# Kernel optimization log

Measured on AMD Instinct MI355X. Metric: run time of the kernel, lower is better.

## Reference

```python
import jax, jax.numpy as jnp
import numpy as np

B, T, C = 4, 2048, 1024
H = 16
D = C // H  # head_dim = 64


def setup_inputs() -> dict:
    key = jax.random.key(0)
    k1, k2, k3, k4, k5 = jax.random.split(key, 5)
    s = 1.0 / np.sqrt(C)
    return {
        "x": jax.random.normal(k1, (B, T, C), dtype=jnp.float32),
        "Wqkv": jax.random.normal(k2, (C, 3 * C), dtype=jnp.float32) * s,
        "bqkv": jax.random.normal(k3, (3 * C,), dtype=jnp.float32) * 0.02,
        "Wproj": jax.random.normal(k4, (C, C), dtype=jnp.float32) * s,
        "bproj": jax.random.normal(k5, (C,), dtype=jnp.float32) * 0.02,
    }


def reference(x, Wqkv, bqkv, Wproj, bproj):
    b, t, c = x.shape
    qkv = x @ Wqkv + bqkv                      # [B,T,3C]
    qkv = qkv.reshape(b, t, 3, H, D)
    q, k, v = (qkv[:, :, i].transpose(0, 2, 1, 3) for i in range(3))  # [B,H,T,D]
    scale = D ** -0.5
    attn = jnp.einsum("bhqd,bhkd->bhqk", q, k) * scale
    causal = jnp.tril(jnp.ones((t, t), dtype=bool))
    attn = jnp.where(causal[None, None], attn, -jnp.inf)
    attn = jax.nn.softmax(attn, axis=-1)
    out = jnp.einsum("bhqk,bhkd->bhqd", attn, v)  # [B,H,T,D]
    out = out.transpose(0, 2, 1, 3).reshape(b, t, c)
    return out @ Wproj + bproj
```

## Files before the change

### kernel.cpp

```cpp
#include <hip/hip_runtime.h>
#include <hip/hip_bf16.h>

typedef __bf16 bf16;
typedef __bf16 bf16x4 __attribute__((ext_vector_type(4)));
typedef __bf16 bf16x8 __attribute__((ext_vector_type(8)));
typedef float  f32x4  __attribute__((ext_vector_type(4)));

#define DEV static __device__ __forceinline__

static constexpr int Bsz = 4, T = 2048, C = 1024, H = 16;
static constexpr int M  = Bsz * T;
static constexpr int N1 = 3 * C;
static constexpr float SM_SCALE = 0.125f;

DEV void gload16(const bf16* g, const bf16* l) {
  __builtin_amdgcn_global_load_lds(
      (const __attribute__((address_space(1))) void*)g,
      (__attribute__((address_space(3))) void*)l, 16, 0, 0);
}

__launch_bounds__(256)
__global__ void convert_kernel(const float* __restrict__ in, bf16* __restrict__ out) {
  const size_t i = ((size_t)blockIdx.x * 256 + threadIdx.x) * 8;
  f32x4 a = *(const f32x4*)(in + i);
  f32x4 b = *(const f32x4*)(in + i + 4);
  *(bf16x4*)(out + i)     = __builtin_convertvector(a, bf16x4);
  *(bf16x4*)(out + i + 4) = __builtin_convertvector(b, bf16x4);
}

__launch_bounds__(256)
__global__ void transpose_conv_kernel(const float* __restrict__ in,
                                      bf16* __restrict__ out, int K, int N) {
  __shared__ float t[32][33];
  const int n0 = blockIdx.x * 32, k0 = blockIdx.y * 32;
  const int tx = threadIdx.x & 31, ty = threadIdx.x >> 5;
#pragma unroll
  for (int j = 0; j < 4; ++j)
    t[ty + j * 8][tx] = in[(size_t)(k0 + ty + j * 8) * N + n0 + tx];
  __syncthreads();
#pragma unroll
  for (int j = 0; j < 4; ++j)
    out[(size_t)(n0 + ty + j * 8) * K + k0 + tx] = (bf16)t[tx][ty + j * 8];
}

template <bool OUT_BF16, bool V_SPLIT>
__launch_bounds__(512, 1)
__global__ void gemm8_kernel(const bf16* __restrict__ A,
                             const bf16* __restrict__ Bt,
                             const float* __restrict__ bias,
                             void* __restrict__ Out, bf16* __restrict__ vt,
                             int Ndim, int Kdim) {
  __shared__ bf16 ldsA[3][128 * 64];
  __shared__ bf16 ldsB[3][256 * 64];
  const int tid = threadIdx.x, l = tid & 63, w = tid >> 6;
  const int wm = w >> 2, wn = w & 3;
  const int lr = l & 15, lh = l >> 4;
  const int m0 = blockIdx.x * 128, n0 = blockIdx.y * 256;
  const int rA = tid >> 3, cA = tid & 7;
  const int cs = cA ^ (rA & 7);

  auto STAGE = [&](int nb, int t) {
    const int k0 = t * 64;
#pragma unroll
    for (int i = 0; i < 2; ++i) {
      const int row = i * 64 + rA;
      gload16(A + (size_t)(m0 + row) * Kdim + k0 + cs * 8,
              &ldsA[nb][i * 4096 + w * 512]);
    }
#pragma unroll
    for (int i = 0; i < 4; ++i) {
      const int row = i * 64 + rA;
      gload16(Bt + (size_t)(n0 + row) * Kdim + k0 + cs * 8,
              &ldsB[nb][i * 4096 + w * 512]);
    }
  };

  f32x4 acc[4][4] = {};
  const int NT = Kdim >> 6;

  STAGE(0, 0);
  STAGE(1, 1);
  asm volatile("s_waitcnt vmcnt(6)" ::: "memory");
  __builtin_amdgcn_sched_barrier(0);
  __builtin_amdgcn_s_barrier();
  __builtin_amdgcn_sched_barrier(0);

  for (int t = 0; t < NT; ++t) {
    const int cur = t % 3;
    const bool more = (t + 2) < NT;
    if (more) STAGE((t + 2) % 3, t + 2);
    __builtin_amdgcn_sched_barrier(0);

    const bf16* a_ = &ldsA[cur][0];
    const bf16* b_ = &ldsB[cur][0];
    bf16x8 af[2][4], bfm[2][4];
#pragma unroll
    for (int kk = 0; kk < 2; ++kk) {
#pragma unroll
      for (int mi = 0; mi < 4; ++mi) {
        const int row = wm * 64 + mi * 16 + lr;
        af[kk][mi] = *(const bf16x8*)&a_[row * 64 + (((kk * 4 + lh) ^ (row & 7)) << 3)];
      }
#pragma unroll
      for (int ni = 0; ni < 4; ++ni) {
        const int row = wn * 64 + ni * 16 + lr;
        bfm[kk][ni] = *(const bf16x8*)&b_[row * 64 + (((kk * 4 + lh) ^ (row & 7)) << 3)];
      }
    }
    __builtin_amdgcn_s_setprio(1);
#pragma unroll
    for (int kk = 0; kk < 2; ++kk)
#pragma unroll
      for (int mi = 0; mi < 4; ++mi)
#pragma unroll
        for (int ni = 0; ni < 4; ++ni)
          acc[mi][ni] = __builtin_amdgcn_mfma_f32_16x16x32_bf16(
              af[kk][mi], bfm[kk][ni], acc[mi][ni], 0, 0, 0);
    __builtin_amdgcn_s_setprio(0);
    __builtin_amdgcn_sched_barrier(0);

    if (t + 1 < NT) {
      if (more) {
        asm volatile("s_waitcnt vmcnt(6)" ::: "memory");
      } else {
        asm volatile("s_waitcnt vmcnt(0)" ::: "memory");
      }
      __builtin_amdgcn_sched_barrier(0);
      __builtin_amdgcn_s_barrier();
      __builtin_amdgcn_sched_barrier(0);
    }
  }

  if (V_SPLIT && n0 >= 2 * C) {
    const int b = m0 >> 11, tb = (m0 & 2047) + wm * 64;
#pragma unroll
    for (int ni = 0; ni < 4; ++ni) {
      const int col = n0 - 2 * C + wn * 64 + ni * 16 + lr;
      const int hh = col >> 6, dd = col & 63;
      const float bv = bias[2 * C + col];
      bf16* vdst = vt + ((size_t)((b * H + hh) * 64 + dd)) * T + tb + lh * 4;
#pragma unroll
      for (int mi = 0; mi < 4; ++mi) {
        bf16x4 p4;
#pragma unroll
        for (int r = 0; r < 4; ++r) p4[r] = (bf16)(acc[mi][ni][r] + bv);
        *(bf16x4*)&vdst[mi * 16] = p4;
      }
    }
  } else {
#pragma unroll
    for (int ni = 0; ni < 4; ++ni) {
      const int col = n0 + wn * 64 + ni * 16 + lr;
      const float bv = bias[col];
#pragma unroll
      for (int mi = 0; mi < 4; ++mi) {
#pragma unroll
        for (int r = 0; r < 4; ++r) {
          const int row = m0 + wm * 64 + mi * 16 + lh * 4 + r;
          const float v = acc[mi][ni][r] + bv;
          if (OUT_BF16)
            ((bf16*)Out)[(size_t)row * Ndim + col] = (bf16)v;
          else
            ((float*)Out)[(size_t)row * Ndim + col] = v;
        }
      }
    }
  }
}

DEV int vswz3(int d) { return (d & 7) ^ ((d >> 3) & 7); }

__launch_bounds__(512, 4)
__global__ void attn_kernel(const bf16* __restrict__ qk,
                            const bf16* __restrict__ vt,
                            bf16* __restrict__ out) {
  __shared__ bf16 lds_k[2][128 * 64];
  __shared__ bf16 lds_vt[2][64 * 128];
  __shared__ bf16 lds_p[8][16 * 64];
  const int tid = threadIdx.x, l = tid & 63, w = tid >> 6;
  const int lr = l & 15, lh = l >> 4;
  const int p = blockIdx.x;
  const int bh = p >> 3, jj = p & 7;
  const int b = bh >> 4, h = bh & 15;
  const size_t RS = 2 * C;
  const bf16* base  = qk + (size_t)b * T * RS;
  const bf16* kbase = base + C + h * 64;
  const bf16* vth   = vt + (size_t)bh * 64 * T;
  bf16* op = out + (size_t)b * T * C + h * 64;
  const int r1 = tid >> 3, cc = tid & 7;
  const int kc = cc ^ (r1 & 7);
  const int dV = tid >> 4, cV = tid & 15;

  auto STAGE = [&](int nb, int kt) {
#pragma unroll
    for (int i = 0; i < 2; ++i) {
      const int rowK = i * 64 + r1;
      gload16(kbase + (size_t)(kt * 128 + rowK) * RS + kc * 8,
              &lds_k[nb][i * 4096 + w * 512]);
      const int d = i * 32 + dV;
      const int vc = (cV & 8) | (((cV & 7) ^ vswz3(d)) & 7);
      gload16(vth + (size_t)d * T + kt * 128 + vc * 8,
              &lds_vt[nb][i * 4096 + w * 512]);
    }
  };

  for (int it = 0; it < 2; ++it) {
    const int J = it ? jj : 15 - jj;
    const int q16 = J * 128 + w * 16;
    bf16x8 qf[2];
#pragma unroll
    for (int kk = 0; kk < 2; ++kk) {
      bf16x8 qv = *(const bf16x8*)(base + (size_t)(q16 + lr) * RS + h * 64 + kk * 32 + lh * 8);
#pragma unroll
      for (int j = 0; j < 8; ++j) qf[kk][j] = (bf16)((float)qv[j] * SM_SCALE);
    }

    float mq = -__builtin_inff(), lq = 0.f;
    f32x4 o[4] = {};

    __syncthreads();
    STAGE(0, 0);
    __syncthreads();

    int buf = 0;
    for (int kt = 0; kt <= J; ++kt) {
      const bf16* kb = &lds_k[buf][0];
      const bf16* vb = &lds_vt[buf][0];
      if (kt < J) STAGE(buf ^ 1, kt + 1);

      f32x4 s8[8] = {};
      __builtin_amdgcn_s_setprio(1);
#pragma unroll
      for (int kk = 0; kk < 2; ++kk) {
#pragma unroll
        for (int kn = 0; kn < 8; ++kn) {
          const int key = kn * 16 + lr;
          bf16x8 kf = *(const bf16x8*)&kb[(key * 64 + kk * 32 + lh * 8) ^ ((key & 7) << 3)];
          s8[kn] = __builtin_amdgcn_mfma_f32_16x16x32_bf16(kf, qf[kk], s8[kn], 0, 0, 0);
        }
      }
      __builtin_amdgcn_s_setprio(0);
      if (kt == J) {
        const int qloc = w * 16 + lr;
#pragma unroll
        for (int kn = 0; kn < 8; ++kn)
#pragma unroll
          for (int r = 0; r < 4; ++r)
            if ((kn * 16 + lh * 4 + r) > qloc) s8[kn][r] = -__builtin_inff();
      }
      float pm = s8[0][0];
#pragma unroll
      for (int kn = 0; kn < 8; ++kn)
#pragma unroll
        for (int r = 0; r < 4; ++r) pm = fmaxf(pm, s8[kn][r]);
      pm = fmaxf(pm, __shfl_xor(pm, 16));
      pm = fmaxf(pm, __shfl_xor(pm, 32));
      const float mnew = fmaxf(mq, pm);
      const float alpha_q = __expf(mq - mnew);
      mq = mnew;
      float ssum = 0.f;
#pragma unroll
      for (int kn = 0; kn < 8; ++kn)
#pragma unroll
        for (int r = 0; r < 4; ++r) {
          const float p2 = __expf(s8[kn][r] - mnew);
          s8[kn][r] = p2;
          ssum += p2;
        }
      ssum += __shfl_xor(ssum, 16);
      ssum += __shfl_xor(ssum, 32);
      lq = lq * alpha_q + ssum;
      float al[4];
#pragma unroll
      for (int r = 0; r < 4; ++r) al[r] = __shfl(alpha_q, lh * 4 + r);
#pragma unroll
      for (int ni = 0; ni < 4; ++ni)
#pragma unroll
        for (int r = 0; r < 4; ++r) o[ni][r] *= al[r];
#pragma unroll
      for (int hh = 0; hh < 2; ++hh) {
#pragma unroll
        for (int kn4 = 0; kn4 < 4; ++kn4) {
          const int kn = hh * 4 + kn4;
          bf16x4 pb;
#pragma unroll
          for (int r = 0; r < 4; ++r) pb[r] = (bf16)s8[kn][r];
          *(bf16x4*)&lds_p[w][(lr * 64 + kn4 * 16 + lh * 4) ^ ((lr & 7) << 3)] = pb;
        }
        __builtin_amdgcn_s_setprio(1);
#pragma unroll
        for (int kkl = 0; kkl < 2; ++kkl) {
          bf16x8 pf = *(const bf16x8*)&lds_p[w][(lr * 64 + kkl * 32 + lh * 8) ^ ((lr & 7) << 3)];
#pragma unroll
          for (int ni = 0; ni < 4; ++ni) {
            const int d = ni * 16 + lr;
            const int key = hh * 64 + kkl * 32 + lh * 8;
            bf16x8 vf = *(const bf16x8*)&vb[d * 128 + (key ^ (vswz3(d) << 3))];
            o[ni] = __builtin_amdgcn_mfma_f32_16x16x32_bf16(pf, vf, o[ni], 0, 0, 0);
          }
        }
        __builtin_amdgcn_s_setprio(0);
      }

      if (kt < J) {
        __syncthreads();
        buf ^= 1;
      }
    }
    float lrec[4];
#pragma unroll
    for (int r = 0; r < 4; ++r) lrec[r] = 1.0f / __shfl(lq, lh * 4 + r);
#pragma unroll
    for (int ni = 0; ni < 4; ++ni)
#pragma unroll
      for (int r = 0; r < 4; ++r) {
        const int qrow = q16 + lh * 4 + r;
        op[(size_t)qrow * C + ni * 16 + lr] = (bf16)(o[ni][r] * lrec[r]);
      }
  }
}

extern "C" void kernel_launch(void* const* d_in, const int* in_sizes, int n_in,
                              void* d_out, int out_size, void* d_ws, size_t ws_size,
                              hipStream_t stream) {
  const float* x     = (const float*)d_in[0];
  const float* Wqkv  = (const float*)d_in[1];
  const float* bqkv  = (const float*)d_in[2];
  const float* Wproj = (const float*)d_in[3];
  const float* bproj = (const float*)d_in[4];
  float* out = (float*)d_out;

  char* ws = (char*)d_ws;
  bf16* qk       = (bf16*)(ws);
  bf16* vt       = (bf16*)(ws + 33554432);
  bf16* wqkvt    = (bf16*)(ws + 50331648);
  bf16* wprojt   = (bf16*)(ws + 56623104);
  bf16* attn_out = (bf16*)(ws + 58720256);
  bf16* x_bf16   = attn_out;

  convert_kernel<<<dim3(M * C / (256 * 8)), 256, 0, stream>>>(x, x_bf16);
  transpose_conv_kernel<<<dim3(N1 / 32, C / 32), 256, 0, stream>>>(Wqkv, wqkvt, C, N1);
  transpose_conv_kernel<<<dim3(C / 32, C / 32), 256, 0, stream>>>(Wproj, wprojt, C, C);
  gemm8_kernel<true, true><<<dim3(M / 128, N1 / 256), 512, 0, stream>>>(
      x_bf16, wqkvt, bqkv, qk, vt, 2 * C, C);
  attn_kernel<<<dim3(Bsz * H * 8), 512, 0, stream>>>(qk, vt, attn_out);
  gemm8_kernel<false, false><<<dim3(M / 128, C / 256), 512, 0, stream>>>(
      attn_out, wprojt, bproj, out, nullptr, C, C);
}
```

Measured before the change: 283.7 us.

## Halve GEMM K-tile to raise occupancy and fuse prep kernels into one launch

The GEMM K-tile drops from 64 to 32, which halves LDS per block, changes the swizzle and staging to three loads per thread, and raises the launch bound to allow several blocks per CU. This targets latency hiding through occupancy. It costs twice as many barriers per K and less MFMA work per sync. The three conversion and transpose kernels are merged into one prep kernel to cut launch overhead.

```diff
diff --git a/kernel.cpp b/kernel.cpp
--- a/kernel.cpp
+++ b/kernel.cpp
@@ -20,67 +20,73 @@
 }
 
 __launch_bounds__(256)
-__global__ void convert_kernel(const float* __restrict__ in, bf16* __restrict__ out) {
-  const size_t i = ((size_t)blockIdx.x * 256 + threadIdx.x) * 8;
-  f32x4 a = *(const f32x4*)(in + i);
-  f32x4 b = *(const f32x4*)(in + i + 4);
-  *(bf16x4*)(out + i)     = __builtin_convertvector(a, bf16x4);
-  *(bf16x4*)(out + i + 4) = __builtin_convertvector(b, bf16x4);
-}
-
-__launch_bounds__(256)
-__global__ void transpose_conv_kernel(const float* __restrict__ in,
-                                      bf16* __restrict__ out, int K, int N) {
+__global__ void prep_kernel(const float* __restrict__ x,
+                            const float* __restrict__ Wqkv,
+                            const float* __restrict__ Wproj,
+                            bf16* __restrict__ xb,
+                            bf16* __restrict__ wqkvt,
+                            bf16* __restrict__ wprojt) {
   __shared__ float t[32][33];
-  const int n0 = blockIdx.x * 32, k0 = blockIdx.y * 32;
-  const int tx = threadIdx.x & 31, ty = threadIdx.x >> 5;
+  const int bid = blockIdx.x, tid = threadIdx.x;
+  if (bid < 4096) {
+    const size_t i = ((size_t)bid * 256 + tid) * 8;
+    f32x4 a = *(const f32x4*)(x + i);
+    f32x4 b = *(const f32x4*)(x + i + 4);
+    *(bf16x4*)(xb + i)     = __builtin_convertvector(a, bf16x4);
+    *(bf16x4*)(xb + i + 4) = __builtin_convertvector(b, bf16x4);
+    return;
+  }
+  const float* in;
+  bf16* out;
+  int N, n0, k0;
+  if (bid < 7168) {
+    const int b2 = bid - 4096;
+    in = Wqkv; out = wqkvt; N = N1; n0 = (b2 % 96) * 32; k0 = (b2 / 96) * 32;
+  } else {
+    const int b3 = bid - 7168;
+    in = Wproj; out = wprojt; N = C; n0 = (b3 % 32) * 32; k0 = (b3 / 32) * 32;
+  }
+  const int tx = tid & 31, ty = tid >> 5;
 #pragma unroll
   for (int j = 0; j < 4; ++j)
     t[ty + j * 8][tx] = in[(size_t)(k0 + ty + j * 8) * N + n0 + tx];
   __syncthreads();
 #pragma unroll
   for (int j = 0; j < 4; ++j)
-    out[(size_t)(n0 + ty + j * 8) * K + k0 + tx] = (bf16)t[tx][ty + j * 8];
+    out[(size_t)(n0 + ty + j * 8) * C + k0 + tx] = (bf16)t[tx][ty + j * 8];
 }
 
 template <bool OUT_BF16, bool V_SPLIT>
-__launch_bounds__(512, 1)
+__launch_bounds__(512, 4)
 __global__ void gemm8_kernel(const bf16* __restrict__ A,
                              const bf16* __restrict__ Bt,
                              const float* __restrict__ bias,
                              void* __restrict__ Out, bf16* __restrict__ vt,
                              int Ndim, int Kdim) {
-  __shared__ bf16 ldsA[3][128 * 64];
-  __shared__ bf16 ldsB[3][256 * 64];
+  __shared__ bf16 ldsA[3][128 * 32];
+  __shared__ bf16 ldsB[3][256 * 32];
   const int tid = threadIdx.x, l = tid & 63, w = tid >> 6;
   const int wm = w >> 2, wn = w & 3;
   const int lr = l & 15, lh = l >> 4;
   const int m0 = blockIdx.x * 128, n0 = blockIdx.y * 256;
-  const int rA = tid >> 3, cA = tid & 7;
-  const int cs = cA ^ (rA & 7);
+  const int rS = tid >> 2;
+  const int cs = (tid & 3) ^ ((tid >> 3) & 3);
+  const int fswz = (lr >> 1) & 3;
 
   auto STAGE = [&](int nb, int t) {
-    const int k0 = t * 64;
-#pragma unroll
-    for (int i = 0; i < 2; ++i) {
-      const int row = i * 64 + rA;
-      gload16(A + (size_t)(m0 + row) * Kdim + k0 + cs * 8,
-              &ldsA[nb][i * 4096 + w * 512]);
-    }
-#pragma unroll
-    for (int i = 0; i < 4; ++i) {
-      const int row = i * 64 + rA;
-      gload16(Bt + (size_t)(n0 + row) * Kdim + k0 + cs * 8,
-              &ldsB[nb][i * 4096 + w * 512]);
-    }
+    const int k0 = t * 32;
+    gload16(A  + (size_t)(m0 + rS) * Kdim + k0 + cs * 8, &ldsA[nb][w * 512]);
+    gload16(Bt + (size_t)(n0 + rS) * Kdim + k0 + cs * 8, &ldsB[nb][w * 512]);
+    gload16(Bt + (size_t)(n0 + 128 + rS) * Kdim + k0 + cs * 8,
+            &ldsB[nb][4096 + w * 512]);
   };
 
   f32x4 acc[4][4] = {};
-  const int NT = Kdim >> 6;
+  const int NT = Kdim >> 5;
 
   STAGE(0, 0);
   STAGE(1, 1);
-  asm volatile("s_waitcnt vmcnt(6)" ::: "memory");
+  asm volatile("s_waitcnt vmcnt(3)" ::: "memory");
   __builtin_amdgcn_sched_barrier(0);
   __builtin_amdgcn_s_barrier();
   __builtin_amdgcn_sched_barrier(0);
@@ -93,35 +99,30 @@
 
     const bf16* a_ = &ldsA[cur][0];
     const bf16* b_ = &ldsB[cur][0];
-    bf16x8 af[2][4], bfm[2][4];
-#pragma unroll
-    for (int kk = 0; kk < 2; ++kk) {
-#pragma unroll
-      for (int mi = 0; mi < 4; ++mi) {
-        const int row = wm * 64 + mi * 16 + lr;
-        af[kk][mi] = *(const bf16x8*)&a_[row * 64 + (((kk * 4 + lh) ^ (row & 7)) << 3)];
-      }
-#pragma unroll
-      for (int ni = 0; ni < 4; ++ni) {
-        const int row = wn * 64 + ni * 16 + lr;
-        bfm[kk][ni] = *(const bf16x8*)&b_[row * 64 + (((kk * 4 + lh) ^ (row & 7)) << 3)];
-      }
+    bf16x8 af[4], bfm[4];
+#pragma unroll
+    for (int mi = 0; mi < 4; ++mi) {
+      const int row = wm * 64 + mi * 16 + lr;
+      af[mi] = *(const bf16x8*)&a_[row * 32 + ((lh ^ fswz) << 3)];
+    }
+#pragma unroll
+    for (int ni = 0; ni < 4; ++ni) {
+      const int row = wn * 64 + ni * 16 + lr;
+      bfm[ni] = *(const bf16x8*)&b_[row * 32 + ((lh ^ fswz) << 3)];
     }
     __builtin_amdgcn_s_setprio(1);
 #pragma unroll
-    for (int kk = 0; kk < 2; ++kk)
-#pragma unroll
-      for (int mi = 0; mi < 4; ++mi)
-#pragma unroll
-        for (int ni = 0; ni < 4; ++ni)
-          acc[mi][ni] = __builtin_amdgcn_mfma_f32_16x16x32_bf16(
-              af[kk][mi], bfm[kk][ni], acc[mi][ni], 0, 0, 0);
+    for (int mi = 0; mi < 4; ++mi)
+#pragma unroll
+      for (int ni = 0; ni < 4; ++ni)
+        acc[mi][ni] = __builtin_amdgcn_mfma_f32_16x16x32_bf16(
+            af[mi], bfm[ni], acc[mi][ni], 0, 0, 0);
     __builtin_amdgcn_s_setprio(0);
     __builtin_amdgcn_sched_barrier(0);
 
     if (t + 1 < NT) {
       if (more) {
-        asm volatile("s_waitcnt vmcnt(6)" ::: "memory");
+        asm volatile("s_waitcnt vmcnt(3)" ::: "memory");
       } else {
         asm volatile("s_waitcnt vmcnt(0)" ::: "memory");
       }
@@ -338,9 +339,7 @@
   bf16* attn_out = (bf16*)(ws + 58720256);
   bf16* x_bf16   = attn_out;
 
-  convert_kernel<<<dim3(M * C / (256 * 8)), 256, 0, stream>>>(x, x_bf16);
-  transpose_conv_kernel<<<dim3(N1 / 32, C / 32), 256, 0, stream>>>(Wqkv, wqkvt, C, N1);
-  transpose_conv_kernel<<<dim3(C / 32, C / 32), 256, 0, stream>>>(Wproj, wprojt, C, C);
+  prep_kernel<<<dim3(8192), 256, 0, stream>>>(x, Wqkv, Wproj, x_bf16, wqkvt, wprojt);
   gemm8_kernel<true, true><<<dim3(M / 128, N1 / 256), 512, 0, stream>>>(
       x_bf16, wqkvt, bqkv, qk, vt, 2 * C, C);
   attn_kernel<<<dim3(Bsz * H * 8), 512, 0, stream>>>(qk, vt, attn_out);
```

Result: no change. 280.7 us (-1.1%).
